# Kernel tuning notes

Hardware: AMD Instinct MI355X
Metric: run time of the kernel (lower is better)

## Reference

```python
import jax, jax.numpy as jnp
import numpy as np

N = 100_000      # nodes
E = 3_200_000    # edges (avg degree 32)
F_IN = 100       # raw feature dim (embedding Linear(100, 64))
H = 64           # in/hidden/out channels
C = 18           # class_num
EPS = 1e-12      # F.normalize eps


def _sage_conv(x, src, dst, edge_weight, Wl, bl, Wr):
    """PyG-style SAGEConv: mean-aggregate neighbor messages, two linears, L2 normalize."""
    msg = x[src]                                   # [E, d] gather of x_j
    if edge_weight is not None:
        msg = msg * edge_weight[:, None]
    agg = jax.ops.segment_sum(msg, dst, num_segments=N)                       # [N, d]
    deg = jax.ops.segment_sum(jnp.ones((src.shape[0],), x.dtype), dst, num_segments=N)
    mean = agg / jnp.maximum(deg, 1.0)[:, None]
    out = mean @ Wl + bl + x @ Wr                  # lin_l(aggr) + lin_r(root)
    nrm = jnp.sqrt(jnp.sum(out * out, axis=-1, keepdims=True))
    return out / jnp.maximum(nrm, EPS)


def setup_inputs() -> dict:
    key = jax.random.key(0)
    ks = jax.random.split(key, 16)
    s = 0.1
    inp = {
        "x": jax.random.normal(ks[0], (N, F_IN), jnp.float32),
        "edge_index": jax.random.randint(ks[1], (2, E), 0, N, dtype=jnp.int64),
        "edge_weight": jax.random.uniform(ks[2], (E,), jnp.float32),
        "emb_W": jax.random.normal(ks[3], (F_IN, H), jnp.float32) * s,
        "emb_b": jnp.zeros((H,), jnp.float32),
    }
    k = 4
    for i in (1, 2, 3):
        inp[f"Wl{i}"] = jax.random.normal(ks[k], (H, H), jnp.float32) * s; k += 1
        inp[f"bl{i}"] = jnp.zeros((H,), jnp.float32)
        inp[f"Wr{i}"] = jax.random.normal(ks[k], (H, H), jnp.float32) * s; k += 1
    inp["Wl4"] = jax.random.normal(ks[k], (H, C), jnp.float32) * s; k += 1
    inp["bl4"] = jnp.zeros((C,), jnp.float32)
    inp["Wr4"] = jax.random.normal(ks[k], (H, C), jnp.float32) * s
    return inp


def reference(x, edge_index, edge_weight, emb_W, emb_b,
              Wl1, bl1, Wr1, Wl2, bl2, Wr2, Wl3, bl3, Wr3,
              Wl4, bl4, Wr4):
    src, dst = edge_index[0], edge_index[1]
    h = jax.nn.relu(x @ emb_W + emb_b)             # embedding MLP
    for Wl, bl, Wr in ((Wl1, bl1, Wr1), (Wl2, bl2, Wr2), (Wl3, bl3, Wr3)):
        h = jax.nn.relu(_sage_conv(h, src, dst, edge_weight, Wl, bl, Wr))
        # dropout p=0.2 is identity in eval mode
    return _sage_conv(h, src, dst, None, Wl4, bl4, Wr4)
```

## Files before the change

kernel.cpp:

```cpp
#include <hip/hip_runtime.h>
#include <hip/hip_bf16.h>

#define N_NODES   100000
#define N_EDGES   3200000
#define F_IN      100
#define H_DIM     64
#define C_NUM     18
#define NPB       1024
#define N_BKT     98
#define EPB       8192
#define N_TILES   1563

typedef __attribute__((ext_vector_type(8))) short short8;
typedef __attribute__((ext_vector_type(4))) float f32x4;
typedef __attribute__((ext_vector_type(2))) float f32x2;

__device__ __forceinline__ float ldf(const void* p, long long i, int isbf) {
    if (isbf) return __bfloat162float(((const __hip_bfloat16*)p)[i]);
    return ((const float*)p)[i];
}
__device__ __forceinline__ int ldi(const void* p, long long i, int is64) {
    if (is64) return (int)(((const long long*)p)[i]);
    return ((const int*)p)[i];
}
__device__ __forceinline__ unsigned short f2us(float f) {
    __hip_bfloat16 b = __float2bfloat16(f);
    return *(unsigned short*)&b;
}
__device__ __forceinline__ unsigned char f2fp8(float f) {
    int p = __builtin_amdgcn_cvt_pk_fp8_f32(f, 0.0f, 0, false);
    return (unsigned char)(p & 0xFF);
}

__global__ void detect_kernel(const void* ei, const void* x, int* flags)
{
    if (threadIdx.x != 0 || blockIdx.x != 0) return;
    const long long* e64 = (const long long*)ei;
    int ok64 = 1;
    for (int i = 0; i < 128; ++i) {
        long long v = e64[i];
        if (v < 0 || v >= N_NODES) { ok64 = 0; break; }
    }
    const __hip_bfloat16* xb = (const __hip_bfloat16*)x;
    int cnt = 0;
    for (int i = 0; i < 256; ++i) {
        float v = fabsf(__bfloat162float(xb[i]));
        if (v == 0.0f || (v > 9.5367431640625e-7f && v < 1.0e6f)) ++cnt;
    }
    flags[0] = ok64;
    flags[1] = (cnt >= 240) ? 1 : 0;
}

__global__ void zero98(int* __restrict__ pcnt)
{
    int i = threadIdx.x;
    if (i < N_BKT) pcnt[i] = 0;
}

__global__ __launch_bounds__(1024) void radix_count(const void* ei, int* __restrict__ pcnt,
                                                    const int* __restrict__ flags)
{
    __shared__ int hist[N_BKT];
    const int t = threadIdx.x;
    if (t < N_BKT) hist[t] = 0;
    __syncthreads();
    const int base = blockIdx.x * EPB;
    const int n = min(EPB, N_EDGES - base);
    const int is64 = flags[0];
    for (int j = t; j < n; j += 1024) {
        int d = ldi(ei, (long long)N_EDGES + base + j, is64);
        atomicAdd(&hist[d >> 10], 1);
    }
    __syncthreads();
    if (t < N_BKT) atomicAdd(&pcnt[t], hist[t]);
}

__global__ void scan98(const int* __restrict__ cnt, int* __restrict__ base,
                       int* __restrict__ cursor)
{
    __shared__ int tmp[128];
    const int t = threadIdx.x;
    int v = (t < N_BKT) ? cnt[t] : 0;
    tmp[t] = v;
    __syncthreads();
    for (int off = 1; off < 128; off <<= 1) {
        int add = (t >= off) ? tmp[t - off] : 0;
        __syncthreads();
        tmp[t] += add;
        __syncthreads();
    }
    if (t < N_BKT) { base[t] = tmp[t] - v; cursor[t] = tmp[t] - v; }
    if (t == 127) base[N_BKT] = tmp[127];
}

__global__ __launch_bounds__(1024) void radix_scatter(const void* ei, const void* ew,
                                                      int* __restrict__ gcursor,
                                                      uint2* __restrict__ temp,
                                                      const int* __restrict__ flags)
{
    __shared__ uint2 stage[EPB];
    __shared__ unsigned char stgb[EPB];
    __shared__ int hist[128], scan_s[128];
    __shared__ int gbase[N_BKT], lcur[N_BKT];
    const int t = threadIdx.x;
    if (t < 128) hist[t] = 0;
    __syncthreads();

    const int base = blockIdx.x * EPB;
    const int n = min(EPB, N_EDGES - base);
    const int is64 = flags[0], isbf = flags[1];

    int  bkt[8];
    uint2 pk[8];
#pragma unroll
    for (int j = 0; j < 8; ++j) {
        int i = j * 1024 + t;
        bkt[j] = -1;
        if (i < n) {
            int e = base + i;
            int s = ldi(ei, e, is64);
            int d = ldi(ei, (long long)N_EDGES + e, is64);
            float w = ldf(ew, e, isbf);
            bkt[j] = d >> 10;
            pk[j].x = (unsigned)s | ((unsigned)(d & (NPB - 1)) << 17);
            pk[j].y = (unsigned)f2us(w);
            atomicAdd(&hist[bkt[j]], 1);
        }
    }
    __syncthreads();
    if (t < 128) scan_s[t] = hist[t];
    __syncthreads();
    for (int off = 1; off < 128; off <<= 1) {
        int add = 0;
        if (t < 128 && t >= off) add = scan_s[t - off];
        __syncthreads();
        if (t < 128) scan_s[t] += add;
        __syncthreads();
    }
    if (t < N_BKT) {
        int excl = scan_s[t] - hist[t];
        lcur[t] = excl;
        gbase[t] = atomicAdd(&gcursor[t], hist[t]) - excl;
    }
    __syncthreads();
#pragma unroll
    for (int j = 0; j < 8; ++j) {
        if (bkt[j] >= 0) {
            int pos = atomicAdd(&lcur[bkt[j]], 1);
            stage[pos] = pk[j];
            stgb[pos] = (unsigned char)bkt[j];
        }
    }
    __syncthreads();
#pragma unroll
    for (int j = 0; j < 8; ++j) {
        int i = j * 1024 + t;
        if (i < n) {
            int b = stgb[i];
            temp[gbase[b] + i] = stage[i];
        }
    }
}

__global__ __launch_bounds__(1024) void csr_build(const uint2* __restrict__ temp,
                          const int* __restrict__ pbase,
                          unsigned int* __restrict__ csr_pk,
                          int* __restrict__ deg, int* __restrict__ row_start,
                          float* __restrict__ inv_deg)
{
    __shared__ int cnt[NPB], scan_s[NPB], cur[NPB];
    const int b = blockIdx.x;
    const int t = threadIdx.x;
    cnt[t] = 0;
    __syncthreads();
    const int bs = pbase[b];
    const int be = pbase[b + 1];
    for (int i = bs + t; i < be; i += NPB)
        atomicAdd(&cnt[(temp[i].x >> 17) & (NPB - 1)], 1);
    __syncthreads();
    int v = cnt[t];
    scan_s[t] = v;
    __syncthreads();
    for (int off = 1; off < NPB; off <<= 1) {
        int add = (t >= off) ? scan_s[t - off] : 0;
        __syncthreads();
        scan_s[t] += add;
        __syncthreads();
    }
    int excl = bs + scan_s[t] - v;
    cur[t] = excl;
    int node = b * NPB + t;
    if (node < N_NODES) {
        deg[node]       = v;
        row_start[node] = excl;
        inv_deg[node]   = 1.0f / (float)max(v, 1);
    }
    __syncthreads();
    for (int i = bs + t; i < be; i += NPB) {
        uint2 e = temp[i];
        int k = (e.x >> 17) & (NPB - 1);
        int pos = atomicAdd(&cur[k], 1);
        csr_pk[pos] = (e.x & 0x1FFFFu) | ((e.y & 0x7FFFu) << 17);
    }
}

template <int CP, int COUT>
__device__ __forceinline__ void stage_W(unsigned short* W_s, const void* Wl, const void* Wr,
                                        int t, int isbf)
{
    constexpr int KP = 136;
    const int n0 = t >> 3, k8a = t & 7;
    for (int n = n0; n < CP; n += 32) {
#pragma unroll
        for (int hh = 0; hh < 2; ++hh) {
            int k8 = k8a + hh * 8;
            union { unsigned short u[8]; short8 v; } tmp;
#pragma unroll
            for (int j = 0; j < 8; ++j) {
                int k = k8 * 8 + j;
                float val = 0.0f;
                if (n < COUT && k < 128)
                    val = (k < 64) ? ldf(Wl, (long long)k * COUT + n, isbf)
                                   : ldf(Wr, (long long)(k - 64) * COUT + n, isbf);
                tmp.u[j] = f2us(val);
            }
            *(short8*)&W_s[n * KP + k8 * 8] = tmp.v;
        }
    }
}

__global__ void embed_mfma(const void* x, const void* W, const void* b,
                           __hip_bfloat16* __restrict__ h,
                           unsigned char* __restrict__ h8,
                           const int* __restrict__ flags)
{
    constexpr int KP = 136;
    __shared__ unsigned short W_s[H_DIM * KP];
    __shared__ unsigned short x_s[64 * KP];
    __shared__ float b_s[H_DIM];
    const int t = threadIdx.x;
    const int isbf = flags[1];

    {
        const int n0 = t >> 3, k8a = t & 7;
        for (int n = n0; n < H_DIM; n += 32) {
#pragma unroll
            for (int hh = 0; hh < 2; ++hh) {
                int k8 = k8a + hh * 8;
                union { unsigned short u[8]; short8 v; } tmp;
#pragma unroll
                for (int j = 0; j < 8; ++j) {
                    int k = k8 * 8 + j;
                    tmp.u[j] = (k < F_IN) ? f2us(ldf(W, (long long)k * H_DIM + n, isbf))
                                          : (unsigned short)0;
                }
                *(short8*)&W_s[n * KP + k8 * 8] = tmp.v;
            }
        }
    }
    if (t < H_DIM) b_s[t] = ldf(b, t, isbf);
    for (int i = t; i < 64 * 36; i += 256) {
        int row = i / 36, col = 100 + (i % 36);
        x_s[row * KP + col] = 0;
    }

    const int wave = t >> 6, lane = t & 63, c = lane & 15, quad = lane >> 4;

    for (int tile = blockIdx.x; tile < N_TILES; tile += gridDim.x) {
        const int nb0 = tile * 64;
        const int valid = min(64, N_NODES - nb0);
        __syncthreads();
        if (isbf) {
            const uint2* xu = (const uint2*)x + (size_t)nb0 * 25;
            for (int i2 = t; i2 < valid * 25; i2 += 256) {
                int row = i2 / 25, col4 = i2 - row * 25;
                *(uint2*)&x_s[row * KP + col4 * 4] = xu[i2];
            }
        } else {
            for (int i = t; i < valid * 100; i += 256) {
                int row = i / 100, col = i - row * 100;
                x_s[row * KP + col] = f2us(((const float*)x)[(size_t)(nb0 + row) * 100 + col]);
            }
        }
        if (valid < 64) {
            for (int i = t; i < (64 - valid) * 100; i += 256) {
                int row = valid + i / 100, col = i % 100;
                x_s[row * KP + col] = 0;
            }
        }
        __syncthreads();

        short8 bfrag[4][4];
#pragma unroll
        for (int nt = 0; nt < 4; ++nt)
#pragma unroll
            for (int kt = 0; kt < 4; ++kt)
                bfrag[nt][kt] = *(const short8*)&W_s[(nt * 16 + c) * KP + kt * 32 + quad * 8];

        short8 afrag[4];
#pragma unroll
        for (int kt = 0; kt < 4; ++kt)
            afrag[kt] = *(const short8*)&x_s[(wave * 16 + c) * KP + kt * 32 + quad * 8];

        f32x4 acc[4] = {};
#pragma unroll
        for (int nt = 0; nt < 4; ++nt)
#pragma unroll
            for (int kt = 0; kt < 4; ++kt)
                acc[nt] = __builtin_amdgcn_mfma_f32_16x16x32_bf16(afrag[kt], bfrag[nt][kt], acc[nt], 0, 0, 0);

        const int nb = nb0 + wave * 16;
#pragma unroll
        for (int nt = 0; nt < 4; ++nt)
#pragma unroll
            for (int reg = 0; reg < 4; ++reg) {
                int nn = nb + quad * 4 + reg;
                int col = nt * 16 + c;
                if (nn < N_NODES) {
                    float v = fmaxf(acc[nt][reg] + b_s[col], 0.0f);
                    h[(size_t)nn * H_DIM + col] = __float2bfloat16(v);
                    h8[(size_t)nn * H_DIM + col] = f2fp8(v);
                }
            }
    }
}

#define ACC16(HV, W) do {                                                          \
    f32x2 f_;                                                                      \
    f_ = __builtin_amdgcn_cvt_pk_f32_fp8((int)HV.x, false); a[0]=fmaf(W,f_.x,a[0]);  a[1]=fmaf(W,f_.y,a[1]);   \
    f_ = __builtin_amdgcn_cvt_pk_f32_fp8((int)HV.x, true ); a[2]=fmaf(W,f_.x,a[2]);  a[3]=fmaf(W,f_.y,a[3]);   \
    f_ = __builtin_amdgcn_cvt_pk_f32_fp8((int)HV.y, false); a[4]=fmaf(W,f_.x,a[4]);  a[5]=fmaf(W,f_.y,a[5]);   \
    f_ = __builtin_amdgcn_cvt_pk_f32_fp8((int)HV.y, true ); a[6]=fmaf(W,f_.x,a[6]);  a[7]=fmaf(W,f_.y,a[7]);   \
    f_ = __builtin_amdgcn_cvt_pk_f32_fp8((int)HV.z, false); a[8]=fmaf(W,f_.x,a[8]);  a[9]=fmaf(W,f_.y,a[9]);   \
    f_ = __builtin_amdgcn_cvt_pk_f32_fp8((int)HV.z, true ); a[10]=fmaf(W,f_.x,a[10]); a[11]=fmaf(W,f_.y,a[11]); \
    f_ = __builtin_amdgcn_cvt_pk_f32_fp8((int)HV.w, false); a[12]=fmaf(W,f_.x,a[12]); a[13]=fmaf(W,f_.y,a[13]); \
    f_ = __builtin_amdgcn_cvt_pk_f32_fp8((int)HV.w, true ); a[14]=fmaf(W,f_.x,a[14]); a[15]=fmaf(W,f_.y,a[15]); \
} while (0)

template <bool USE_W>
__global__ __launch_bounds__(256) void gather_mean(const unsigned char* __restrict__ h8,
                            const unsigned int* __restrict__ csr_pk,
                            const int* __restrict__ row_start,
                            const int* __restrict__ deg,
                            const float* __restrict__ inv_deg,
                            __hip_bfloat16* __restrict__ mean)
{
    const int lane = threadIdx.x & 63;
    const int c4 = lane & 3;
    const int r4 = lane >> 2;
    const int wid = blockIdx.x * 4 + (threadIdx.x >> 6);
    const int nw  = gridDim.x * 4;

    for (int n = wid; n < N_NODES; n += nw) {
        const int s0 = row_start[n];
        const int d0 = deg[n];
        unsigned int ev = (lane < d0) ? csr_pk[s0 + lane] : 0u;
        const int m0 = min(d0, 64);
        float a[16] = {};

        for (int j0 = 0; j0 < m0; j0 += 32) {
            unsigned int eA = __shfl(ev, j0 + r4);
            unsigned int eB = __shfl(ev, j0 + 16 + r4);
            uint4 hvA = *(const uint4*)(h8 + (size_t)(eA & 0x1FFFF) * H_DIM + 16 * c4);
            uint4 hvB = *(const uint4*)(h8 + (size_t)(eB & 0x1FFFF) * H_DIM + 16 * c4);
            float wA, wB;
            if (USE_W) {
                wA = __uint_as_float((eA & 0xFFFE0000u) >> 1);
                wB = __uint_as_float((eB & 0xFFFE0000u) >> 1);
            } else {
                wA = (j0 + r4 < m0) ? 1.0f : 0.0f;
                wB = (j0 + 16 + r4 < m0) ? 1.0f : 0.0f;
            }
            ACC16(hvA, wA);
            ACC16(hvB, wB);
        }
        for (int jb = 64; jb < d0; jb += 16) {
            int j = jb + r4;
            unsigned int e2 = (j < d0) ? csr_pk[s0 + j] : 0u;
            float w;
            if (USE_W) w = __uint_as_float((e2 & 0xFFFE0000u) >> 1);
            else       w = (j < d0) ? 1.0f : 0.0f;
            uint4 hv = *(const uint4*)(h8 + (size_t)(e2 & 0x1FFFF) * H_DIM + 16 * c4);
            ACC16(hv, w);
        }

#pragma unroll
        for (int i = 0; i < 8; ++i) {
            float keep = (lane & 4) ? a[i + 8] : a[i];
            float give = (lane & 4) ? a[i] : a[i + 8];
            a[i] = keep + __shfl_xor(give, 4);
        }
#pragma unroll
        for (int i = 0; i < 4; ++i) {
            float keep = (lane & 8) ? a[i + 4] : a[i];
            float give = (lane & 8) ? a[i] : a[i + 4];
            a[i] = keep + __shfl_xor(give, 8);
        }
#pragma unroll
        for (int i = 0; i < 2; ++i) {
            float keep = (lane & 16) ? a[i + 2] : a[i];
            float give = (lane & 16) ? a[i] : a[i + 2];
            a[i] = keep + __shfl_xor(give, 16);
        }
        {
            float keep = (lane & 32) ? a[1] : a[0];
            float give = (lane & 32) ? a[0] : a[1];
            a[0] = keep + __shfl_xor(give, 32);
        }
        const int f = c4 * 16 + ((lane >> 2) & 1) * 8 + ((lane >> 3) & 1) * 4
                    + ((lane >> 4) & 1) * 2 + ((lane >> 5) & 1);
        mean[(size_t)n * H_DIM + f] = __float2bfloat16(a[0] * inv_deg[n]);
    }
}

template <int COUT, bool RELU, bool FINAL>
__global__ void transform_mfma(const __hip_bfloat16* __restrict__ meanp,
                               const __hip_bfloat16* __restrict__ hp,
                               const void* Wl, const void* bl, const void* Wr,
                               __hip_bfloat16* __restrict__ h_out,
                               unsigned char* __restrict__ h8_out,
                               const int* __restrict__ flags, void* dout)
{
    constexpr int CP = (COUT + 15) & ~15;
    constexpr int NT = CP / 16;
    constexpr int KP = 136;
    __shared__ unsigned short W_s[CP * KP];
    __shared__ float b_s[CP];
    const int t = threadIdx.x;
    const int isbf = flags[1];
    stage_W<CP, COUT>(W_s, Wl, Wr, t, isbf);
    if (t < CP) b_s[t] = (t < COUT) ? ldf(bl, t, isbf) : 0.0f;
    __syncthreads();

    const int wave = t >> 6, lane = t & 63, c = lane & 15, quad = lane >> 4;
    short8 bfrag[NT][4];
#pragma unroll
    for (int nt = 0; nt < NT; ++nt)
#pragma unroll
        for (int kt = 0; kt < 4; ++kt)
            bfrag[nt][kt] = *(const short8*)&W_s[(nt * 16 + c) * KP + kt * 32 + quad * 8];

    for (int tile = blockIdx.x; tile < N_TILES; tile += gridDim.x) {
        const int nbw = tile * 64 + wave * 16;
        if (nbw >= N_NODES) continue;
        int node = nbw + c; if (node >= N_NODES) node = N_NODES - 1;

        short8 afrag[4];
#pragma unroll
        for (int kt = 0; kt < 4; ++kt) {
            const __hip_bfloat16* sp = (kt < 2) ? meanp : hp;
            afrag[kt] = *(const short8*)(sp + (size_t)node * H_DIM + (kt & 1) * 32 + quad * 8);
        }

        f32x4 acc[NT] = {};
#pragma unroll
        for (int nt = 0; nt < NT; ++nt)
#pragma unroll
            for (int kt = 0; kt < 4; ++kt)
                acc[nt] = __builtin_amdgcn_mfma_f32_16x16x32_bf16(afrag[kt], bfrag[nt][kt], acc[nt], 0, 0, 0);

        float rs[4];
#pragma unroll
        for (int reg = 0; reg < 4; ++reg) {
            float s2 = 0.f;
#pragma unroll
            for (int nt = 0; nt < NT; ++nt) {
                float v = acc[nt][reg] + b_s[nt * 16 + c];
                acc[nt][reg] = v;
                s2 += v * v;
            }
            s2 += __shfl_xor(s2, 1); s2 += __shfl_xor(s2, 2);
            s2 += __shfl_xor(s2, 4); s2 += __shfl_xor(s2, 8);
            rs[reg] = 1.0f / fmaxf(sqrtf(s2), 1e-12f);
        }

#pragma unroll
        for (int nt = 0; nt < NT; ++nt)
#pragma unroll
            for (int reg = 0; reg < 4; ++reg) {
                int nn  = nbw + quad * 4 + reg;
                int col = nt * 16 + c;
                if (nn < N_NODES && col < COUT) {
                    float v = acc[nt][reg] * rs[reg];
                    if (RELU) v = fmaxf(v, 0.0f);
                    if (FINAL) {
                        if (isbf) ((__hip_bfloat16*)dout)[(size_t)nn * COUT + col] = __float2bfloat16(v);
                        else      ((float*)dout)[(size_t)nn * COUT + col] = v;
                    } else {
                        h_out[(size_t)nn * H_DIM + col] = __float2bfloat16(v);
                        h8_out[(size_t)nn * H_DIM + col] = f2fp8(v);
                    }
                }
            }
    }
}

extern "C" void kernel_launch(void* const* d_in, const int* in_sizes, int n_in,
                              void* d_out, int out_size, void* d_ws, size_t ws_size,
                              hipStream_t stream)
{
    const void* x    = d_in[0];
    const void* ei   = d_in[1];
    const void* ew   = d_in[2];
    const void* embW = d_in[3];
    const void* embB = d_in[4];
    const void* Wl1 = d_in[5];  const void* bl1 = d_in[6];  const void* Wr1 = d_in[7];
    const void* Wl2 = d_in[8];  const void* bl2 = d_in[9];  const void* Wr2 = d_in[10];
    const void* Wl3 = d_in[11]; const void* bl3 = d_in[12]; const void* Wr3 = d_in[13];
    const void* Wl4 = d_in[14]; const void* bl4 = d_in[15]; const void* Wr4 = d_in[16];
    (void)in_sizes; (void)n_in; (void)out_size; (void)ws_size;

    char* ws = (char*)d_ws;
    size_t off = 0;
    auto alloc = [&](size_t bytes) -> void* {
        void* p = ws + off;
        off += (bytes + 255) & ~(size_t)255;
        return p;
    };
    uint2* temp = (uint2*)alloc((size_t)N_EDGES * sizeof(uint2));
    __hip_bfloat16* hA = (__hip_bfloat16*)temp;
    __hip_bfloat16* hB = (__hip_bfloat16*)((char*)temp + (size_t)N_NODES * H_DIM * 2);
    unsigned int* csr_pk = (unsigned int*)alloc((size_t)N_EDGES * sizeof(unsigned int));
    __hip_bfloat16* mn = (__hip_bfloat16*)alloc((size_t)N_NODES * H_DIM * 2);
    unsigned char* h8 = (unsigned char*)alloc((size_t)N_NODES * H_DIM);
    int*   pcnt    = (int*)  alloc((N_BKT)     * sizeof(int));
    int*   pbase   = (int*)  alloc((N_BKT + 1) * sizeof(int));
    int*   pcursor = (int*)  alloc((N_BKT)     * sizeof(int));
    int*   deg     = (int*)  alloc((size_t)N_NODES * sizeof(int));
    int*   row_st  = (int*)  alloc((size_t)N_NODES * sizeof(int));
    float* inv_deg = (float*)alloc((size_t)N_NODES * sizeof(float));
    int*   flags   = (int*)  alloc(256);

    const int NBr = (N_EDGES + EPB - 1) / EPB;

    detect_kernel<<<1, 64, 0, stream>>>(ei, x, flags);
    zero98<<<1, 128, 0, stream>>>(pcnt);
    radix_count<<<NBr, 1024, 0, stream>>>(ei, pcnt, flags);
    scan98<<<1, 128, 0, stream>>>(pcnt, pbase, pcursor);
    radix_scatter<<<NBr, 1024, 0, stream>>>(ei, ew, pcursor, temp, flags);
    csr_build<<<N_BKT, NPB, 0, stream>>>(temp, pbase, csr_pk, deg, row_st, inv_deg);

    embed_mfma<<<512, 256, 0, stream>>>(x, embW, embB, hA, h8, flags);

    gather_mean<true><<<2048, 256, 0, stream>>>(h8, csr_pk, row_st, deg, inv_deg, mn);
    transform_mfma<H_DIM, true, false><<<512, 256, 0, stream>>>(
        mn, hA, Wl1, bl1, Wr1, hB, h8, flags, d_out);
    gather_mean<true><<<2048, 256, 0, stream>>>(h8, csr_pk, row_st, deg, inv_deg, mn);
    transform_mfma<H_DIM, true, false><<<512, 256, 0, stream>>>(
        mn, hB, Wl2, bl2, Wr2, hA, h8, flags, d_out);
    gather_mean<true><<<2048, 256, 0, stream>>>(h8, csr_pk, row_st, deg, inv_deg, mn);
    transform_mfma<H_DIM, true, false><<<512, 256, 0, stream>>>(
        mn, hA, Wl3, bl3, Wr3, hB, h8, flags, d_out);
    gather_mean<false><<<2048, 256, 0, stream>>>(h8, csr_pk, row_st, deg, inv_deg, mn);
    transform_mfma<C_NUM, false, true><<<512, 256, 0, stream>>>(
        mn, hB, Wl4, bl4, Wr4, nullptr, nullptr, flags, d_out);
}
```

Baseline: 545.9 us.

## Split fp8 features into two 32-column planes and shrink CSR buckets

Stores the fp8 node features as two planes of 32 columns each. Each gather block now processes only one plane, with each lane reading 16 bytes and two lanes covering a row. This halves the per-edge gather footprint, so each plane's working set (about 3.2MB) is more likely to stay in cache. Radix buckets shrink from 1024 to 256 nodes (391 buckets), the bucket id is packed into the staged edge word instead of a separate byte array, and csr_build runs with 256 threads. The cost is that every edge list is read twice, once per plane, along with more buckets and a longer scan.

```diff
diff --git a/kernel.cpp b/kernel.cpp
--- a/kernel.cpp
+++ b/kernel.cpp
@@ -6,14 +6,16 @@
 #define F_IN      100
 #define H_DIM     64
 #define C_NUM     18
-#define NPB       1024
-#define N_BKT     98
+#define NPB       256
+#define N_BKT     391
 #define EPB       8192
 #define N_TILES   1563
 
 typedef __attribute__((ext_vector_type(8))) short short8;
 typedef __attribute__((ext_vector_type(4))) float f32x4;
 typedef __attribute__((ext_vector_type(2))) float f32x2;
+
+#define PLANE_SZ ((size_t)N_NODES * 32)
 
 __device__ __forceinline__ float ldf(const void* p, long long i, int isbf) {
     if (isbf) return __bfloat162float(((const __hip_bfloat16*)p)[i]);
@@ -51,7 +53,7 @@
     flags[1] = (cnt >= 240) ? 1 : 0;
 }
 
-__global__ void zero98(int* __restrict__ pcnt)
+__global__ void zero_cnt(int* __restrict__ pcnt)
 {
     int i = threadIdx.x;
     if (i < N_BKT) pcnt[i] = 0;
@@ -69,28 +71,28 @@
     const int is64 = flags[0];
     for (int j = t; j < n; j += 1024) {
         int d = ldi(ei, (long long)N_EDGES + base + j, is64);
-        atomicAdd(&hist[d >> 10], 1);
+        atomicAdd(&hist[d >> 8], 1);
     }
     __syncthreads();
     if (t < N_BKT) atomicAdd(&pcnt[t], hist[t]);
 }
 
-__global__ void scan98(const int* __restrict__ cnt, int* __restrict__ base,
-                       int* __restrict__ cursor)
-{
-    __shared__ int tmp[128];
+__global__ void scan_bkt(const int* __restrict__ cnt, int* __restrict__ base,
+                         int* __restrict__ cursor)
+{
+    __shared__ int tmp[512];
     const int t = threadIdx.x;
     int v = (t < N_BKT) ? cnt[t] : 0;
     tmp[t] = v;
     __syncthreads();
-    for (int off = 1; off < 128; off <<= 1) {
+    for (int off = 1; off < 512; off <<= 1) {
         int add = (t >= off) ? tmp[t - off] : 0;
         __syncthreads();
         tmp[t] += add;
         __syncthreads();
     }
     if (t < N_BKT) { base[t] = tmp[t] - v; cursor[t] = tmp[t] - v; }
-    if (t == 127) base[N_BKT] = tmp[127];
+    if (t == 511) base[N_BKT] = tmp[511];
 }
 
 __global__ __launch_bounds__(1024) void radix_scatter(const void* ei, const void* ew,
@@ -99,11 +101,10 @@
                                                       const int* __restrict__ flags)
 {
     __shared__ uint2 stage[EPB];
-    __shared__ unsigned char stgb[EPB];
-    __shared__ int hist[128], scan_s[128];
+    __shared__ int hist[512], scan_s[512];
     __shared__ int gbase[N_BKT], lcur[N_BKT];
     const int t = threadIdx.x;
-    if (t < 128) hist[t] = 0;
+    if (t < 512) hist[t] = 0;
     __syncthreads();
 
     const int base = blockIdx.x * EPB;
@@ -121,20 +122,20 @@
             int s = ldi(ei, e, is64);
             int d = ldi(ei, (long long)N_EDGES + e, is64);
             float w = ldf(ew, e, isbf);
-            bkt[j] = d >> 10;
+            bkt[j] = d >> 8;
             pk[j].x = (unsigned)s | ((unsigned)(d & (NPB - 1)) << 17);
-            pk[j].y = (unsigned)f2us(w);
+            pk[j].y = (unsigned)f2us(w) | ((unsigned)bkt[j] << 16);
             atomicAdd(&hist[bkt[j]], 1);
         }
     }
     __syncthreads();
-    if (t < 128) scan_s[t] = hist[t];
-    __syncthreads();
-    for (int off = 1; off < 128; off <<= 1) {
+    if (t < 512) scan_s[t] = hist[t];
+    __syncthreads();
+    for (int off = 1; off < 512; off <<= 1) {
         int add = 0;
-        if (t < 128 && t >= off) add = scan_s[t - off];
-        __syncthreads();
-        if (t < 128) scan_s[t] += add;
+        if (t < 512 && t >= off) add = scan_s[t - off];
+        __syncthreads();
+        if (t < 512) scan_s[t] += add;
         __syncthreads();
     }
     if (t < N_BKT) {
@@ -148,7 +149,6 @@
         if (bkt[j] >= 0) {
             int pos = atomicAdd(&lcur[bkt[j]], 1);
             stage[pos] = pk[j];
-            stgb[pos] = (unsigned char)bkt[j];
         }
     }
     __syncthreads();
@@ -156,13 +156,13 @@
     for (int j = 0; j < 8; ++j) {
         int i = j * 1024 + t;
         if (i < n) {
-            int b = stgb[i];
+            int b = (int)(stage[i].y >> 16);
             temp[gbase[b] + i] = stage[i];
         }
     }
 }
 
-__global__ __launch_bounds__(1024) void csr_build(const uint2* __restrict__ temp,
+__global__ __launch_bounds__(256) void csr_build(const uint2* __restrict__ temp,
                           const int* __restrict__ pbase,
                           unsigned int* __restrict__ csr_pk,
                           int* __restrict__ deg, int* __restrict__ row_start,
@@ -319,7 +319,7 @@
                 if (nn < N_NODES) {
                     float v = fmaxf(acc[nt][reg] + b_s[col], 0.0f);
                     h[(size_t)nn * H_DIM + col] = __float2bfloat16(v);
-                    h8[(size_t)nn * H_DIM + col] = f2fp8(v);
+                    h8[(size_t)(col >> 5) * PLANE_SZ + (size_t)nn * 32 + (col & 31)] = f2fp8(v);
                 }
             }
     }
@@ -346,10 +346,14 @@
                             __hip_bfloat16* __restrict__ mean)
 {
     const int lane = threadIdx.x & 63;
-    const int c4 = lane & 3;
-    const int r4 = lane >> 2;
-    const int wid = blockIdx.x * 4 + (threadIdx.x >> 6);
-    const int nw  = gridDim.x * 4;
+    const int c2 = lane & 1;
+    const int r2 = lane >> 1;
+    const int bid = blockIdx.x;
+    const int plane = (bid >> 2) & 1;
+    const int pb = ((bid >> 3) << 2) | (bid & 3);
+    const int wid = pb * 4 + (threadIdx.x >> 6);
+    const int nw  = (gridDim.x >> 1) * 4;
+    const unsigned char* hp = h8 + (size_t)plane * PLANE_SZ;
 
     for (int n = wid; n < N_NODES; n += nw) {
         const int s0 = row_start[n];
@@ -359,57 +363,53 @@
         float a[16] = {};
 
         for (int j0 = 0; j0 < m0; j0 += 32) {
-            unsigned int eA = __shfl(ev, j0 + r4);
-            unsigned int eB = __shfl(ev, j0 + 16 + r4);
-            uint4 hvA = *(const uint4*)(h8 + (size_t)(eA & 0x1FFFF) * H_DIM + 16 * c4);
-            uint4 hvB = *(const uint4*)(h8 + (size_t)(eB & 0x1FFFF) * H_DIM + 16 * c4);
-            float wA, wB;
-            if (USE_W) {
-                wA = __uint_as_float((eA & 0xFFFE0000u) >> 1);
-                wB = __uint_as_float((eB & 0xFFFE0000u) >> 1);
-            } else {
-                wA = (j0 + r4 < m0) ? 1.0f : 0.0f;
-                wB = (j0 + 16 + r4 < m0) ? 1.0f : 0.0f;
-            }
-            ACC16(hvA, wA);
-            ACC16(hvB, wB);
-        }
-        for (int jb = 64; jb < d0; jb += 16) {
-            int j = jb + r4;
+            unsigned int e = __shfl(ev, j0 + r2);
+            uint4 hv = *(const uint4*)(hp + (size_t)(e & 0x1FFFF) * 32 + 16 * c2);
+            float w;
+            if (USE_W) w = __uint_as_float((e & 0xFFFE0000u) >> 1);
+            else       w = (j0 + r2 < m0) ? 1.0f : 0.0f;
+            ACC16(hv, w);
+        }
+        for (int jb = 64; jb < d0; jb += 32) {
+            int j = jb + r2;
             unsigned int e2 = (j < d0) ? csr_pk[s0 + j] : 0u;
             float w;
             if (USE_W) w = __uint_as_float((e2 & 0xFFFE0000u) >> 1);
             else       w = (j < d0) ? 1.0f : 0.0f;
-            uint4 hv = *(const uint4*)(h8 + (size_t)(e2 & 0x1FFFF) * H_DIM + 16 * c4);
+            uint4 hv = *(const uint4*)(hp + (size_t)(e2 & 0x1FFFF) * 32 + 16 * c2);
             ACC16(hv, w);
         }
 
 #pragma unroll
         for (int i = 0; i < 8; ++i) {
-            float keep = (lane & 4) ? a[i + 8] : a[i];
-            float give = (lane & 4) ? a[i] : a[i + 8];
+            float keep = (lane & 2) ? a[i + 8] : a[i];
+            float give = (lane & 2) ? a[i] : a[i + 8];
+            a[i] = keep + __shfl_xor(give, 2);
+        }
+#pragma unroll
+        for (int i = 0; i < 4; ++i) {
+            float keep = (lane & 4) ? a[i + 4] : a[i];
+            float give = (lane & 4) ? a[i] : a[i + 4];
             a[i] = keep + __shfl_xor(give, 4);
         }
 #pragma unroll
-        for (int i = 0; i < 4; ++i) {
-            float keep = (lane & 8) ? a[i + 4] : a[i];
-            float give = (lane & 8) ? a[i] : a[i + 4];
+        for (int i = 0; i < 2; ++i) {
+            float keep = (lane & 8) ? a[i + 2] : a[i];
+            float give = (lane & 8) ? a[i] : a[i + 2];
             a[i] = keep + __shfl_xor(give, 8);
         }
-#pragma unroll
-        for (int i = 0; i < 2; ++i) {
-            float keep = (lane & 16) ? a[i + 2] : a[i];
-            float give = (lane & 16) ? a[i] : a[i + 2];
-            a[i] = keep + __shfl_xor(give, 16);
-        }
         {
-            float keep = (lane & 32) ? a[1] : a[0];
-            float give = (lane & 32) ? a[0] : a[1];
-            a[0] = keep + __shfl_xor(give, 32);
-        }
-        const int f = c4 * 16 + ((lane >> 2) & 1) * 8 + ((lane >> 3) & 1) * 4
-                    + ((lane >> 4) & 1) * 2 + ((lane >> 5) & 1);
-        mean[(size_t)n * H_DIM + f] = __float2bfloat16(a[0] * inv_deg[n]);
+            float keep = (lane & 16) ? a[1] : a[0];
+            float give = (lane & 16) ? a[0] : a[1];
+            a[0] = keep + __shfl_xor(give, 16);
+        }
+        a[0] += __shfl_xor(a[0], 32);
+
+        if (!(lane & 32)) {
+            const int f = c2 * 16 + ((lane >> 1) & 1) * 8 + ((lane >> 2) & 1) * 4
+                        + ((lane >> 3) & 1) * 2 + ((lane >> 4) & 1);
+            mean[(size_t)n * H_DIM + plane * 32 + f] = __float2bfloat16(a[0] * inv_deg[n]);
+        }
     }
 }
 
@@ -488,7 +488,7 @@
                         else      ((float*)dout)[(size_t)nn * COUT + col] = v;
                     } else {
                         h_out[(size_t)nn * H_DIM + col] = __float2bfloat16(v);
-                        h8_out[(size_t)nn * H_DIM + col] = f2fp8(v);
+                        h8_out[(size_t)(col >> 5) * PLANE_SZ + (size_t)nn * 32 + (col & 31)] = f2fp8(v);
                     }
                 }
             }
@@ -534,9 +534,9 @@
     const int NBr = (N_EDGES + EPB - 1) / EPB;
 
     detect_kernel<<<1, 64, 0, stream>>>(ei, x, flags);
-    zero98<<<1, 128, 0, stream>>>(pcnt);
+    zero_cnt<<<1, 512, 0, stream>>>(pcnt);
     radix_count<<<NBr, 1024, 0, stream>>>(ei, pcnt, flags);
-    scan98<<<1, 128, 0, stream>>>(pcnt, pbase, pcursor);
+    scan_bkt<<<1, 512, 0, stream>>>(pcnt, pbase, pcursor);
     radix_scatter<<<NBr, 1024, 0, stream>>>(ei, ew, pcursor, temp, flags);
     csr_build<<<N_BKT, NPB, 0, stream>>>(temp, pbase, csr_pk, deg, row_st, inv_deg);
 
```

Result: slower. 565.4 us (+3.6%).

## Use finer 256-node buckets for CSR build and parallelize detection

Applied to the files above, without the earlier changes.

Shrinks the radix bucket width from 1024 to 256 destination nodes, giving 391 buckets so csr_build launches more, smaller blocks that spread across the GPU. The bucket id is packed into the high bits of the weight word, which removes the separate byte staging array in radix_scatter. The format detection kernel now runs across a full wavefront with ballot and shuffle reductions instead of a single serial thread. The scans now span 512 entries and scatter writes go to more distinct regions, which adds some overhead in the radix passes.

```diff
diff --git a/kernel.cpp b/kernel.cpp
--- a/kernel.cpp
+++ b/kernel.cpp
@@ -6,8 +6,8 @@
 #define F_IN      100
 #define H_DIM     64
 #define C_NUM     18
-#define NPB       1024
-#define N_BKT     98
+#define NPB       256
+#define N_BKT     391
 #define EPB       8192
 #define N_TILES   1563
 
@@ -34,24 +34,32 @@
 
 __global__ void detect_kernel(const void* ei, const void* x, int* flags)
 {
-    if (threadIdx.x != 0 || blockIdx.x != 0) return;
+    if (blockIdx.x != 0 || threadIdx.x >= 64) return;
+    const int lane = threadIdx.x;
     const long long* e64 = (const long long*)ei;
-    int ok64 = 1;
-    for (int i = 0; i < 128; ++i) {
+    int bad = 0;
+#pragma unroll
+    for (int i = lane; i < 128; i += 64) {
         long long v = e64[i];
-        if (v < 0 || v >= N_NODES) { ok64 = 0; break; }
-    }
+        if (v < 0 || v >= N_NODES) bad = 1;
+    }
+    unsigned long long anybad = __ballot(bad);
     const __hip_bfloat16* xb = (const __hip_bfloat16*)x;
     int cnt = 0;
-    for (int i = 0; i < 256; ++i) {
+#pragma unroll
+    for (int i = lane; i < 256; i += 64) {
         float v = fabsf(__bfloat162float(xb[i]));
         if (v == 0.0f || (v > 9.5367431640625e-7f && v < 1.0e6f)) ++cnt;
     }
-    flags[0] = ok64;
-    flags[1] = (cnt >= 240) ? 1 : 0;
-}
-
-__global__ void zero98(int* __restrict__ pcnt)
+#pragma unroll
+    for (int m = 1; m <= 32; m <<= 1) cnt += __shfl_xor(cnt, m);
+    if (lane == 0) {
+        flags[0] = (anybad == 0ULL) ? 1 : 0;
+        flags[1] = (cnt >= 240) ? 1 : 0;
+    }
+}
+
+__global__ void zero_cnt(int* __restrict__ pcnt)
 {
     int i = threadIdx.x;
     if (i < N_BKT) pcnt[i] = 0;
@@ -69,28 +77,28 @@
     const int is64 = flags[0];
     for (int j = t; j < n; j += 1024) {
         int d = ldi(ei, (long long)N_EDGES + base + j, is64);
-        atomicAdd(&hist[d >> 10], 1);
+        atomicAdd(&hist[d >> 8], 1);
     }
     __syncthreads();
     if (t < N_BKT) atomicAdd(&pcnt[t], hist[t]);
 }
 
-__global__ void scan98(const int* __restrict__ cnt, int* __restrict__ base,
-                       int* __restrict__ cursor)
-{
-    __shared__ int tmp[128];
+__global__ void scan_bkt(const int* __restrict__ cnt, int* __restrict__ base,
+                         int* __restrict__ cursor)
+{
+    __shared__ int tmp[512];
     const int t = threadIdx.x;
     int v = (t < N_BKT) ? cnt[t] : 0;
     tmp[t] = v;
     __syncthreads();
-    for (int off = 1; off < 128; off <<= 1) {
+    for (int off = 1; off < 512; off <<= 1) {
         int add = (t >= off) ? tmp[t - off] : 0;
         __syncthreads();
         tmp[t] += add;
         __syncthreads();
     }
     if (t < N_BKT) { base[t] = tmp[t] - v; cursor[t] = tmp[t] - v; }
-    if (t == 127) base[N_BKT] = tmp[127];
+    if (t == 511) base[N_BKT] = tmp[511];
 }
 
 __global__ __launch_bounds__(1024) void radix_scatter(const void* ei, const void* ew,
@@ -99,11 +107,10 @@
                                                       const int* __restrict__ flags)
 {
     __shared__ uint2 stage[EPB];
-    __shared__ unsigned char stgb[EPB];
-    __shared__ int hist[128], scan_s[128];
+    __shared__ int hist[512], scan_s[512];
     __shared__ int gbase[N_BKT], lcur[N_BKT];
     const int t = threadIdx.x;
-    if (t < 128) hist[t] = 0;
+    if (t < 512) hist[t] = 0;
     __syncthreads();
 
     const int base = blockIdx.x * EPB;
@@ -121,20 +128,20 @@
             int s = ldi(ei, e, is64);
             int d = ldi(ei, (long long)N_EDGES + e, is64);
             float w = ldf(ew, e, isbf);
-            bkt[j] = d >> 10;
+            bkt[j] = d >> 8;
             pk[j].x = (unsigned)s | ((unsigned)(d & (NPB - 1)) << 17);
-            pk[j].y = (unsigned)f2us(w);
+            pk[j].y = (unsigned)f2us(w) | ((unsigned)bkt[j] << 16);
             atomicAdd(&hist[bkt[j]], 1);
         }
     }
     __syncthreads();
-    if (t < 128) scan_s[t] = hist[t];
-    __syncthreads();
-    for (int off = 1; off < 128; off <<= 1) {
+    if (t < 512) scan_s[t] = hist[t];
+    __syncthreads();
+    for (int off = 1; off < 512; off <<= 1) {
         int add = 0;
-        if (t < 128 && t >= off) add = scan_s[t - off];
-        __syncthreads();
-        if (t < 128) scan_s[t] += add;
+        if (t < 512 && t >= off) add = scan_s[t - off];
+        __syncthreads();
+        if (t < 512) scan_s[t] += add;
         __syncthreads();
     }
     if (t < N_BKT) {
@@ -148,7 +155,6 @@
         if (bkt[j] >= 0) {
             int pos = atomicAdd(&lcur[bkt[j]], 1);
             stage[pos] = pk[j];
-            stgb[pos] = (unsigned char)bkt[j];
         }
     }
     __syncthreads();
@@ -156,13 +162,13 @@
     for (int j = 0; j < 8; ++j) {
         int i = j * 1024 + t;
         if (i < n) {
-            int b = stgb[i];
+            int b = (int)(stage[i].y >> 16);
             temp[gbase[b] + i] = stage[i];
         }
     }
 }
 
-__global__ __launch_bounds__(1024) void csr_build(const uint2* __restrict__ temp,
+__global__ __launch_bounds__(256) void csr_build(const uint2* __restrict__ temp,
                           const int* __restrict__ pbase,
                           unsigned int* __restrict__ csr_pk,
                           int* __restrict__ deg, int* __restrict__ row_start,
@@ -534,9 +540,9 @@
     const int NBr = (N_EDGES + EPB - 1) / EPB;
 
     detect_kernel<<<1, 64, 0, stream>>>(ei, x, flags);
-    zero98<<<1, 128, 0, stream>>>(pcnt);
+    zero_cnt<<<1, 512, 0, stream>>>(pcnt);
     radix_count<<<NBr, 1024, 0, stream>>>(ei, pcnt, flags);
-    scan98<<<1, 128, 0, stream>>>(pcnt, pbase, pcursor);
+    scan_bkt<<<1, 512, 0, stream>>>(pcnt, pbase, pcursor);
     radix_scatter<<<NBr, 1024, 0, stream>>>(ei, ew, pcursor, temp, flags);
     csr_build<<<N_BKT, NPB, 0, stream>>>(temp, pbase, csr_pk, deg, row_st, inv_deg);
 
```

After: 520.6 us. 1.05x faster.
